# Kernel optimization log

Measured on AMD Instinct MI355X. Metric: run time of the kernel, lower is better.

The kernel has to match this reference:

```python
import jax, jax.numpy as jnp
import numpy as np

M, K, N = 4096, 4096, 11008  # tokens, in_features, out_features


def setup_inputs() -> dict:
    key = jax.random.key(0)
    k0, k1, k2 = jax.random.split(key, 3)
    # quint8 activations: values in [0, 255], zero_point 128
    x_q = jax.random.randint(k0, (M, K), 0, 256, dtype=jnp.int32)
    # qint8 weight: values in [-128, 127], zero_point 0 (as prepacked in __init__)
    w_q = jax.random.randint(k1, (N, K), -128, 128, dtype=jnp.int32)
    bias = jax.random.normal(k2, (N,), dtype=jnp.float32) * 0.1
    return {
        "x_q": x_q,
        "w_q": w_q,
        "bias": bias,
        "x_scale": jnp.float32(0.02),
        "w_scale": jnp.float32(0.01),
        "out_scale": jnp.float32(1.0),   # self.scale = 1.0
        "x_zero_point": 128,
        "out_zero_point": 0,             # self.zero_point = 0
    }


def reference(x_q, w_q, bias, x_scale, w_scale, out_scale, x_zero_point, out_zero_point):
    # int8 GEMM with int32 accumulation: (x - zp_x) @ W^T
    acc = jnp.einsum(
        "mk,nk->mn",
        x_q - x_zero_point,
        w_q,
        preferred_element_type=jnp.int32,
    )
    # dequantize + bias (fp32), then requantize to quint8 output
    y = acc.astype(jnp.float32) * (x_scale * w_scale) + bias
    q = jnp.clip(jnp.round(y / out_scale) + out_zero_point, 0, 255).astype(jnp.int32)
    return q
```

## Files before the change

kernel.cpp:

```cpp
#include <hip/hip_runtime.h>

#define M_DIM 4096
#define K_DIM 4096
#define N_DIM 11008
#define BM 128
#define BN 128
#define BK 128

typedef int v4i __attribute__((ext_vector_type(4)));

__device__ __forceinline__ void load_lds16(const void* g, void* l) {
    __builtin_amdgcn_global_load_lds(
        (const __attribute__((address_space(1))) void*)g,
        (__attribute__((address_space(3))) void*)l,
        16, 0, 0);
}

__global__ void pack_x_kernel(const int* __restrict__ x, signed char* __restrict__ out,
                              const int* __restrict__ zp_p, int n4) {
    int i = blockIdx.x * blockDim.x + threadIdx.x;
    if (i >= n4) return;
    int zp = zp_p[0];
    int4 v = ((const int4*)x)[i];
    unsigned int p = ((unsigned int)(v.x - zp) & 0xFF)
                   | (((unsigned int)(v.y - zp) & 0xFF) << 8)
                   | (((unsigned int)(v.z - zp) & 0xFF) << 16)
                   | (((unsigned int)(v.w - zp) & 0xFF) << 24);
    ((unsigned int*)out)[i] = p;
}

__global__ void pack_w_kernel(const int* __restrict__ w, signed char* __restrict__ out, int n4) {
    int i = blockIdx.x * blockDim.x + threadIdx.x;
    if (i >= n4) return;
    int4 v = ((const int4*)w)[i];
    unsigned int p = ((unsigned int)v.x & 0xFF)
                   | (((unsigned int)v.y & 0xFF) << 8)
                   | (((unsigned int)v.z & 0xFF) << 16)
                   | (((unsigned int)v.w & 0xFF) << 24);
    ((unsigned int*)out)[i] = p;
}

__global__ __launch_bounds__(256) void gemm_i8_kernel(
    const signed char* __restrict__ A8,
    const signed char* __restrict__ B8,
    const float* __restrict__ bias,
    const float* __restrict__ xs_p, const float* __restrict__ ws_p,
    const float* __restrict__ os_p, const int* __restrict__ ozp_p,
    int* __restrict__ out) {
    __shared__ v4i As[BM * BK / 16];
    __shared__ v4i Bs[BN * BK / 16];

    const int tid  = threadIdx.x;
    const int lane = tid & 63;
    const int wave = tid >> 6;

    const int bid   = blockIdx.x;
    const int xcd   = bid & 7;
    const int local = bid >> 3;
    const int m_blk = xcd * 4 + (local & 3);
    const int n_blk = (local >> 4) * 4 + ((local & 15) >> 2);
    const int m0 = m_blk * BM;
    const int n0 = n_blk * BN;

    long offA[4], offB[4];
    char *ldsA[4], *ldsB[4];
#pragma unroll
    for (int j = 0; j < 4; ++j) {
        const int s   = tid + 256 * j;
        const int row = s >> 3;
        const int gg  = (s & 7) ^ (row & 7);
        offA[j] = (long)(m0 + row) * K_DIM + gg * 16;
        offB[j] = (long)(n0 + row) * K_DIM + gg * 16;
        ldsA[j] = (char*)As + s * 16;
        ldsB[j] = (char*)Bs + s * 16;
    }

    const int waveM = wave >> 1, waveN = wave & 1;
    const int l15 = lane & 15, quad = lane >> 4;
    int aSlot[4][2], bSlot[4][2];
#pragma unroll
    for (int t = 0; t < 4; ++t) {
#pragma unroll
        for (int ks = 0; ks < 2; ++ks) {
            const int g = ks * 4 + quad;
            aSlot[t][ks] = (waveM * 64 + t * 16 + l15) * 8 + (g ^ (l15 & 7));
            bSlot[t][ks] = (waveN * 64 + t * 16 + l15) * 8 + (g ^ (l15 & 7));
        }
    }

    v4i acc[4][4];
#pragma unroll
    for (int mt = 0; mt < 4; ++mt)
#pragma unroll
        for (int nt = 0; nt < 4; ++nt) {
            v4i z = {0, 0, 0, 0};
            acc[mt][nt] = z;
        }

    for (int k0 = 0; k0 < K_DIM; k0 += BK) {
#pragma unroll
        for (int j = 0; j < 4; ++j) load_lds16(A8 + offA[j] + k0, ldsA[j]);
#pragma unroll
        for (int j = 0; j < 4; ++j) load_lds16(B8 + offB[j] + k0, ldsB[j]);
        __syncthreads();

#pragma unroll
        for (int ks = 0; ks < 2; ++ks) {
            v4i a[4], b[4];
#pragma unroll
            for (int t = 0; t < 4; ++t) a[t] = As[aSlot[t][ks]];
#pragma unroll
            for (int t = 0; t < 4; ++t) b[t] = Bs[bSlot[t][ks]];
#pragma unroll
            for (int mt = 0; mt < 4; ++mt)
#pragma unroll
                for (int nt = 0; nt < 4; ++nt)
                    acc[mt][nt] = __builtin_amdgcn_mfma_i32_16x16x64_i8(
                        a[mt], b[nt], acc[mt][nt], 0, 0, 0);
        }
        __syncthreads();
    }

    const float scale  = xs_p[0] * ws_p[0];
    const float inv_os = 1.0f / os_p[0];
    const int   ozp    = ozp_p[0];
#pragma unroll
    for (int mt = 0; mt < 4; ++mt) {
        const int rbase = m0 + waveM * 64 + mt * 16 + quad * 4;
#pragma unroll
        for (int nt = 0; nt < 4; ++nt) {
            const int col = n0 + waveN * 64 + nt * 16 + l15;
            const float bv = bias[col];
#pragma unroll
            for (int r = 0; r < 4; ++r) {
                float y = (float)acc[mt][nt][r] * scale + bv;
                int q = (int)rintf(y * inv_os) + ozp;
                q = q < 0 ? 0 : (q > 255 ? 255 : q);
                out[(long)(rbase + r) * N_DIM + col] = q;
            }
        }
    }
}

extern "C" void kernel_launch(void* const* d_in, const int* in_sizes, int n_in,
                              void* d_out, int out_size, void* d_ws, size_t ws_size,
                              hipStream_t stream) {
    const int*   x_q  = (const int*)d_in[0];
    const int*   w_q  = (const int*)d_in[1];
    const float* bias = (const float*)d_in[2];
    const float* xs   = (const float*)d_in[3];
    const float* wsc  = (const float*)d_in[4];
    const float* os   = (const float*)d_in[5];
    const int*   xzp  = (const int*)d_in[6];
    const int*   ozp  = (const int*)d_in[7];

    signed char* x8 = (signed char*)d_ws;
    signed char* w8 = (signed char*)d_ws + (size_t)M_DIM * K_DIM;

    const int nx4 = M_DIM * K_DIM / 4;
    pack_x_kernel<<<(nx4 + 255) / 256, 256, 0, stream>>>(x_q, x8, xzp, nx4);
    const int nw4 = N_DIM * K_DIM / 4;
    pack_w_kernel<<<(nw4 + 255) / 256, 256, 0, stream>>>(w_q, w8, nw4);

    const int nblocks = (M_DIM / BM) * (N_DIM / BN);
    gemm_i8_kernel<<<nblocks, 256, 0, stream>>>(x8, w8, bias, xs, wsc, os, ozp, (int*)d_out);
}
```

Measured before the change: 565.9 us.

## Double-buffer LDS tiles and switch to 32x32x32 int8 MFMA

Adds a second LDS buffer pair so global-to-LDS loads for the next K tile are issued while the current tile is computed, with explicit vmcnt waits and barriers replacing the per-iteration syncthreads. The inner product also moves from 16x16x64 to 32x32x32 int8 MFMA tiles, which cuts the number of LDS fragment reads per MFMA. The epilogue is remapped to the 32x32 accumulator layout. LDS use doubles to 64KB per block, which may lower occupancy, and the hand-coded waitcnt values must match the number of outstanding loads.

Result: faster. 519.7 us (-8.2%).

```diff
diff --git a/kernel.cpp b/kernel.cpp
--- a/kernel.cpp
+++ b/kernel.cpp
@@ -6,8 +6,13 @@
 #define BM 128
 #define BN 128
 #define BK 128
+#define NTILES (K_DIM / BK)
 
-typedef int v4i __attribute__((ext_vector_type(4)));
+typedef int v4i  __attribute__((ext_vector_type(4)));
+typedef int v16i __attribute__((ext_vector_type(16)));
+
+#define WAIT_VM8 0x3F78
+#define WAIT_VM0 0x3F70
 
 __device__ __forceinline__ void load_lds16(const void* g, void* l) {
     __builtin_amdgcn_global_load_lds(
@@ -47,8 +52,10 @@
     const float* __restrict__ xs_p, const float* __restrict__ ws_p,
     const float* __restrict__ os_p, const int* __restrict__ ozp_p,
     int* __restrict__ out) {
-    __shared__ v4i As[BM * BK / 16];
-    __shared__ v4i Bs[BN * BK / 16];
+    __shared__ v4i As0[BM * BK / 16];
+    __shared__ v4i Bs0[BN * BK / 16];
+    __shared__ v4i As1[BM * BK / 16];
+    __shared__ v4i Bs1[BN * BK / 16];
 
     const int tid  = threadIdx.x;
     const int lane = tid & 63;
@@ -63,80 +70,105 @@
     const int n0 = n_blk * BN;
 
     long offA[4], offB[4];
-    char *ldsA[4], *ldsB[4];
+    int  ldsOff[4];
 #pragma unroll
     for (int j = 0; j < 4; ++j) {
         const int s   = tid + 256 * j;
         const int row = s >> 3;
         const int gg  = (s & 7) ^ (row & 7);
-        offA[j] = (long)(m0 + row) * K_DIM + gg * 16;
-        offB[j] = (long)(n0 + row) * K_DIM + gg * 16;
-        ldsA[j] = (char*)As + s * 16;
-        ldsB[j] = (char*)Bs + s * 16;
+        offA[j]   = (long)(m0 + row) * K_DIM + gg * 16;
+        offB[j]   = (long)(n0 + row) * K_DIM + gg * 16;
+        ldsOff[j] = s;
     }
 
     const int waveM = wave >> 1, waveN = wave & 1;
-    const int l15 = lane & 15, quad = lane >> 4;
-    int aSlot[4][2], bSlot[4][2];
+    const int l31 = lane & 31, h = lane >> 5;
+    int aSlot[2][4], bSlot[2][4];
 #pragma unroll
-    for (int t = 0; t < 4; ++t) {
+    for (int t = 0; t < 2; ++t) {
+        const int rA = waveM * 64 + t * 32 + l31;
+        const int rB = waveN * 64 + t * 32 + l31;
 #pragma unroll
-        for (int ks = 0; ks < 2; ++ks) {
-            const int g = ks * 4 + quad;
-            aSlot[t][ks] = (waveM * 64 + t * 16 + l15) * 8 + (g ^ (l15 & 7));
-            bSlot[t][ks] = (waveN * 64 + t * 16 + l15) * 8 + (g ^ (l15 & 7));
+        for (int s = 0; s < 4; ++s) {
+            const int g = 2 * s + h;
+            aSlot[t][s] = rA * 8 + (g ^ (rA & 7));
+            bSlot[t][s] = rB * 8 + (g ^ (rB & 7));
         }
     }
 
-    v4i acc[4][4];
+    v16i acc[2][2];
 #pragma unroll
-    for (int mt = 0; mt < 4; ++mt)
+    for (int mt = 0; mt < 2; ++mt)
 #pragma unroll
-        for (int nt = 0; nt < 4; ++nt) {
-            v4i z = {0, 0, 0, 0};
-            acc[mt][nt] = z;
-        }
+        for (int nt = 0; nt < 2; ++nt)
+#pragma unroll
+            for (int r = 0; r < 16; ++r) acc[mt][nt][r] = 0;
 
-    for (int k0 = 0; k0 < K_DIM; k0 += BK) {
+    auto stage = [&](int tile, v4i* Asb, v4i* Bsb) {
+        const long koff = (long)tile * BK;
 #pragma unroll
-        for (int j = 0; j < 4; ++j) load_lds16(A8 + offA[j] + k0, ldsA[j]);
+        for (int j = 0; j < 4; ++j) load_lds16(A8 + offA[j] + koff, (char*)(Asb + ldsOff[j]));
 #pragma unroll
-        for (int j = 0; j < 4; ++j) load_lds16(B8 + offB[j] + k0, ldsB[j]);
-        __syncthreads();
-
+        for (int j = 0; j < 4; ++j) load_lds16(B8 + offB[j] + koff, (char*)(Bsb + ldsOff[j]));
+    };
+    auto compute = [&](const v4i* Asb, const v4i* Bsb) {
 #pragma unroll
-        for (int ks = 0; ks < 2; ++ks) {
-            v4i a[4], b[4];
+        for (int s = 0; s < 4; ++s) {
+            v4i a[2], b[2];
 #pragma unroll
-            for (int t = 0; t < 4; ++t) a[t] = As[aSlot[t][ks]];
+            for (int t = 0; t < 2; ++t) a[t] = Asb[aSlot[t][s]];
 #pragma unroll
-            for (int t = 0; t < 4; ++t) b[t] = Bs[bSlot[t][ks]];
+            for (int t = 0; t < 2; ++t) b[t] = Bsb[bSlot[t][s]];
 #pragma unroll
-            for (int mt = 0; mt < 4; ++mt)
+            for (int mt = 0; mt < 2; ++mt)
 #pragma unroll
-                for (int nt = 0; nt < 4; ++nt)
-                    acc[mt][nt] = __builtin_amdgcn_mfma_i32_16x16x64_i8(
+                for (int nt = 0; nt < 2; ++nt)
+                    acc[mt][nt] = __builtin_amdgcn_mfma_i32_32x32x32_i8(
                         a[mt], b[nt], acc[mt][nt], 0, 0, 0);
         }
-        __syncthreads();
+    };
+
+    stage(0, As0, Bs0);
+    stage(1, As1, Bs1);
+
+#pragma unroll 1
+    for (int kk = 0; kk < 15; ++kk) {
+        const int k = 2 * kk;
+        __builtin_amdgcn_s_waitcnt(WAIT_VM8);
+        __builtin_amdgcn_s_barrier();
+        compute(As0, Bs0);
+        __builtin_amdgcn_s_barrier();
+        stage(k + 2, As0, Bs0);
+        __builtin_amdgcn_s_waitcnt(WAIT_VM8);
+        __builtin_amdgcn_s_barrier();
+        compute(As1, Bs1);
+        __builtin_amdgcn_s_barrier();
+        stage(k + 3, As1, Bs1);
     }
+    __builtin_amdgcn_s_waitcnt(WAIT_VM8);
+    __builtin_amdgcn_s_barrier();
+    compute(As0, Bs0);
+    __builtin_amdgcn_s_waitcnt(WAIT_VM0);
+    __builtin_amdgcn_s_barrier();
+    compute(As1, Bs1);
 
     const float scale  = xs_p[0] * ws_p[0];
     const float inv_os = 1.0f / os_p[0];
     const int   ozp    = ozp_p[0];
 #pragma unroll
-    for (int mt = 0; mt < 4; ++mt) {
-        const int rbase = m0 + waveM * 64 + mt * 16 + quad * 4;
+    for (int mt = 0; mt < 2; ++mt) {
+        const int rbase = m0 + waveM * 64 + mt * 32 + 4 * h;
 #pragma unroll
-        for (int nt = 0; nt < 4; ++nt) {
-            const int col = n0 + waveN * 64 + nt * 16 + l15;
+        for (int nt = 0; nt < 2; ++nt) {
+            const int col = n0 + waveN * 64 + nt * 32 + l31;
             const float bv = bias[col];
 #pragma unroll
-            for (int r = 0; r < 4; ++r) {
+            for (int r = 0; r < 16; ++r) {
+                const int row = rbase + (r & 3) + 8 * (r >> 2);
                 float y = (float)acc[mt][nt][r] * scale + bv;
                 int q = (int)rintf(y * inv_os) + ozp;
                 q = q < 0 ? 0 : (q > 255 ? 255 : q);
-                out[(long)(rbase + r) * N_DIM + col] = q;
+                out[(long)row * N_DIM + col] = q;
             }
         }
     }
```
